# Performance work log

Measured on AMD Instinct MI355X. Metric: run time of the kernel, lower is better.

Reference implementation:

```python
import jax, jax.numpy as jnp
import numpy as np

P_MASKING = 0.065
MASKING_LENGTH = 10

B, T, D = 16, 4096, 768


def setup_inputs() -> dict:
    key = jax.random.key(0)
    k1, k2, k3 = jax.random.split(key, 3)
    x = jax.random.normal(k1, (B, T, D), dtype=jnp.float32)
    mask_token = jax.random.normal(k2, (D,), dtype=jnp.float32)
    rand_vals = jax.random.uniform(k3, (B, T), dtype=jnp.float32)
    return {"x": x, "mask_token": mask_token, "rand_vals": rand_vals}


def _span_mask(rand_vals: jnp.ndarray) -> jnp.ndarray:
    """Positions covered by any masked span of length MASKING_LENGTH.

    Position j is masked iff there is a start at some i in (j-L, j].
    Computed with a cumsum difference instead of the original per-span
    Python-loop scatter writes.
    """
    start_pos = (rand_vals < P_MASKING).astype(jnp.int32)   # [B, T]
    c = jnp.cumsum(start_pos, axis=1)                        # [B, T]
    c_shift = jnp.pad(c, ((0, 0), (MASKING_LENGTH, 0)))[:, : c.shape[1]]
    return (c - c_shift) > 0                                 # bool [B, T]


def reference(x, mask_token, rand_vals):
    # Faithful vectorized version of D2VEncoder.mask_tokens:
    #   x[i, j:j+L, :] = mask_token ; mask[i, j:j+L] = -inf for each start (i,j)
    masked = _span_mask(rand_vals)                           # [B, T]
    x_out = jnp.where(masked[:, :, None], mask_token[None, None, :], x)
    mask = jnp.where(masked, -jnp.inf, 0.0).astype(x.dtype)  # [B, T]
    return x_out, mask
```

## Files before the change

kernel.cpp:

```cpp
#include <hip/hip_runtime.h>

#define P_MASKING 0.065f
#define MASK_LEN 10
#define MASK_NEG_BIG (-1.0e38f)

constexpr int B = 16;
constexpr int T = 4096;
constexpr int D = 768;
constexpr int DV = D / 4;
constexpr int NROWS = B * T;
constexpr unsigned NVEC = (unsigned)NROWS * DV;

__global__ void d2v_v5_flags_mask(unsigned char* __restrict__ flags,
                                  float* __restrict__ mask_out,
                                  const float* __restrict__ rand_vals) {
    int idx = blockIdx.x * blockDim.x + threadIdx.x;
    if (idx >= NROWS) return;
    int t = idx & (T - 1);
    int base = idx - t;
    int lo = t - (MASK_LEN - 1);
    if (lo < 0) lo = 0;
    bool m = false;
    for (int i = lo; i <= t; ++i)
        m |= (rand_vals[base + i] < P_MASKING);
    flags[idx] = m ? (unsigned char)1 : (unsigned char)0;
    mask_out[idx] = m ? MASK_NEG_BIG : 0.0f;
}

__global__ void d2v_v5_fill_x(float4* __restrict__ out,
                              const unsigned char* __restrict__ flags,
                              const float4* __restrict__ x,
                              const float4* __restrict__ token) {
    unsigned stride = gridDim.x * blockDim.x;
    for (unsigned i = blockIdx.x * blockDim.x + threadIdx.x; i < NVEC; i += stride) {
        unsigned row = i / DV;
        unsigned col = i - row * DV;
        float4 v;
        if (flags[row]) {
            v = token[col];
        } else {
            v = x[i];
        }
        out[i] = v;
    }
}

extern "C" void kernel_launch(void* const* d_in, const int* in_sizes, int n_in,
                              void* d_out, int out_size, void* d_ws, size_t ws_size,
                              hipStream_t stream) {
    const float* x         = (const float*)d_in[0];
    const float* token     = (const float*)d_in[1];
    const float* rand_vals = (const float*)d_in[2];

    float* x_out    = (float*)d_out;
    float* mask_out = (float*)d_out + (size_t)NROWS * D;
    unsigned char* flags = (unsigned char*)d_ws;

    {
        int threads = 256;
        int blocks = (NROWS + threads - 1) / threads;
        d2v_v5_flags_mask<<<blocks, threads, 0, stream>>>(flags, mask_out, rand_vals);
    }
    {
        int threads = 256;
        int blocks = 4096;
        d2v_v5_fill_x<<<blocks, threads, 0, stream>>>(
            (float4*)x_out, flags, (const float4*)x, (const float4*)token);
    }
}
```

Baseline: 58.54 us.

## Fuse flag computation and row fill into one wave-per-row kernel

Merges the mask/flag kernel and the copy kernel into one launch where each wavefront handles one row, computing the span flag inline and copying either the token or the x row. This removes the flag buffer round trip, the second launch, and the per-element integer division. It also switches to nontemporal stores for the output. Each lane redundantly recomputes the row flag from rand_vals.

After: 50.27 us. 14.1% less time.

```diff
diff --git a/kernel.cpp b/kernel.cpp
--- a/kernel.cpp
+++ b/kernel.cpp
@@ -9,39 +9,43 @@
 constexpr int D = 768;
 constexpr int DV = D / 4;
 constexpr int NROWS = B * T;
-constexpr unsigned NVEC = (unsigned)NROWS * DV;
 
-__global__ void d2v_v5_flags_mask(unsigned char* __restrict__ flags,
-                                  float* __restrict__ mask_out,
-                                  const float* __restrict__ rand_vals) {
-    int idx = blockIdx.x * blockDim.x + threadIdx.x;
-    if (idx >= NROWS) return;
-    int t = idx & (T - 1);
-    int base = idx - t;
+typedef float f4 __attribute__((ext_vector_type(4)));
+
+__global__ __launch_bounds__(256) void d2v_v7_fused(
+    f4* __restrict__ out,
+    float* __restrict__ mask_out,
+    const f4* __restrict__ x,
+    const f4* __restrict__ token,
+    const float* __restrict__ rand_vals) {
+    int row  = (blockIdx.x << 2) + (threadIdx.x >> 6);
+    int lane = threadIdx.x & 63;
+
+    int t = row & (T - 1);
+    int base = row - t;
     int lo = t - (MASK_LEN - 1);
     if (lo < 0) lo = 0;
     bool m = false;
     for (int i = lo; i <= t; ++i)
         m |= (rand_vals[base + i] < P_MASKING);
-    flags[idx] = m ? (unsigned char)1 : (unsigned char)0;
-    mask_out[idx] = m ? MASK_NEG_BIG : 0.0f;
-}
 
-__global__ void d2v_v5_fill_x(float4* __restrict__ out,
-                              const unsigned char* __restrict__ flags,
-                              const float4* __restrict__ x,
-                              const float4* __restrict__ token) {
-    unsigned stride = gridDim.x * blockDim.x;
-    for (unsigned i = blockIdx.x * blockDim.x + threadIdx.x; i < NVEC; i += stride) {
-        unsigned row = i / DV;
-        unsigned col = i - row * DV;
-        float4 v;
-        if (flags[row]) {
-            v = token[col];
-        } else {
-            v = x[i];
+    if (lane == 0)
+        mask_out[row] = m ? MASK_NEG_BIG : 0.0f;
+
+    f4* orow = out + (size_t)row * DV;
+    if (m) {
+        #pragma unroll
+        for (int j = 0; j < 3; ++j) {
+            f4 v = token[lane + (j << 6)];
+            __builtin_nontemporal_store(v, orow + lane + (j << 6));
         }
-        out[i] = v;
+    } else {
+        const f4* xrow = x + (size_t)row * DV;
+        #pragma unroll
+        for (int j = 0; j < 3; ++j) {
+            f4 v = xrow[lane + (j << 6)];
+            __builtin_nontemporal_store(v, orow + lane + (j << 6));
+        }
     }
 }
 
@@ -54,17 +58,10 @@
 
     float* x_out    = (float*)d_out;
     float* mask_out = (float*)d_out + (size_t)NROWS * D;
-    unsigned char* flags = (unsigned char*)d_ws;
 
-    {
-        int threads = 256;
-        int blocks = (NROWS + threads - 1) / threads;
-        d2v_v5_flags_mask<<<blocks, threads, 0, stream>>>(flags, mask_out, rand_vals);
-    }
-    {
-        int threads = 256;
-        int blocks = 4096;
-        d2v_v5_fill_x<<<blocks, threads, 0, stream>>>(
-            (float4*)x_out, flags, (const float4*)x, (const float4*)token);
-    }
+    int threads = 256;
+    int blocks = NROWS / 4;
+    d2v_v7_fused<<<blocks, threads, 0, stream>>>(
+        (f4*)x_out, mask_out, (const f4*)x, (const f4*)token,
+        rand_vals);
 }
```
